# Optimization experiments

Hardware: AMD Instinct MI355X
Metric: run time of the kernel (lower is better)

Reference implementation:

```python
import jax, jax.numpy as jnp
import numpy as np

VL = 32

def setup_inputs() -> dict:
    key = jax.random.key(0)
    k1, k2, k3 = jax.random.split(key, 3)
    user = jax.random.normal(k1, (16384, 20, VL + 1), dtype=jnp.float32)
    ctx = jax.random.normal(k2, (16384, 10, VL + 1), dtype=jnp.float32)
    doc = jax.random.normal(k3, (16384, 30, VL + 1), dtype=jnp.float32)
    return {"user": user, "ctx": ctx, "doc": doc}

def reference(user, ctx, doc):
    # feats: [B, F, vl+1] where F = total field count across user/ctx/doc
    feats = jnp.concatenate([user, ctx, doc], axis=1)
    v = feats[..., :VL]          # [B, F, vl] latent factors
    linear = feats[..., -1]      # [B, F]   linear term (last column)
    # FM cross term: 0.5 * ((sum_f v)^2 - sum_f v^2), summed over latent dims
    sum_v = jnp.sum(v, axis=1)           # [B, vl]
    sum_v2 = jnp.sum(v * v, axis=1)      # [B, vl]
    cross = 0.5 * jnp.sum(sum_v * sum_v - sum_v2, axis=-1)  # [B]
    logits = cross + jnp.sum(linear, axis=1)                 # [B]
    return jax.nn.sigmoid(logits)
```

## Files before the change

kernel.cpp:

```cpp
#include <hip/hip_runtime.h>
#include <hip/hip_bf16.h>
#include <math.h>


#define NS 16384
#define NU 20
#define NC 10
#define ND 30
#define RW 33

__global__ __launch_bounds__(256) void fm_kernel(
    const float* __restrict__ user,
    const float* __restrict__ ctx,
    const float* __restrict__ doc,
    float* __restrict__ out) {
  const int tid   = blockIdx.x * blockDim.x + threadIdx.x;
  const int samp  = tid >> 5;
  const int lane  = tid & 31;

  const float* __restrict__ ub = user + (size_t)samp * (NU * RW);
  const float* __restrict__ cb = ctx  + (size_t)samp * (NC * RW);
  const float* __restrict__ db = doc  + (size_t)samp * (ND * RW);

  float lin = 0.f;
  if (lane < NU) lin += ub[lane * RW + 32];
  if (lane < NC) lin += cb[lane * RW + 32];
  if (lane < ND) lin += db[lane * RW + 32];

  float sv = 0.f, sv2 = 0.f;

#pragma unroll
  for (int f = 0; f < NU; ++f) {
    float x = ub[f * RW + lane];
    sv += x; sv2 = fmaf(x, x, sv2);
  }
#pragma unroll
  for (int f = 0; f < NC; ++f) {
    float x = cb[f * RW + lane];
    sv += x; sv2 = fmaf(x, x, sv2);
  }
#pragma unroll
  for (int f = 0; f < ND; ++f) {
    float x = db[f * RW + lane];
    sv += x; sv2 = fmaf(x, x, sv2);
  }

  float part = fmaf(sv, sv, -sv2);

#pragma unroll
  for (int m = 16; m > 0; m >>= 1) {
    part += __shfl_xor(part, m, 64);
    lin  += __shfl_xor(lin,  m, 64);
  }

  if (lane == 0) {
    float logit = fmaf(0.5f, part, lin);
    out[samp] = 1.f / (1.f + expf(-logit));
  }
}

extern "C" void kernel_launch(void* const* d_in, const int* in_sizes, int n_in,
                              void* d_out, int out_size, void* d_ws, size_t ws_size,
                              hipStream_t stream) {
  const float* user = (const float*)d_in[0];
  const float* ctx  = (const float*)d_in[1];
  const float* doc  = (const float*)d_in[2];
  float* out = (float*)d_out;

  dim3 block(256);
  dim3 grid(NS / 8);
  fm_kernel<<<grid, block, 0, stream>>>(user, ctx, doc, out);
}
```

Baseline: 153.5 us.

## Stage sample pairs through LDS with coalesced float4 loads per wavefront

Each 64-lane wavefront now handles two samples. It copies their contiguous user/ctx/doc rows into shared memory with aligned float4 loads, then each half-wave reduces one sample from LDS. The aim is to replace the strided 33-float-row global reads with fully coalesced wide loads. The cost is about 31.7 KB of LDS per 128-thread block, which limits occupancy, plus an extra pass through LDS. There is no barrier between the LDS store and load; this relies on each wavefront reading only data it wrote itself.

```diff
diff --git a/kernel.cpp b/kernel.cpp
--- a/kernel.cpp
+++ b/kernel.cpp
@@ -4,46 +4,77 @@
 
 
 #define NS 16384
-#define NU 20
-#define NC 10
-#define ND 30
 #define RW 33
 
-__global__ __launch_bounds__(256) void fm_kernel(
+__global__ __launch_bounds__(128) void fm_kernel(
     const float* __restrict__ user,
     const float* __restrict__ ctx,
     const float* __restrict__ doc,
     float* __restrict__ out) {
-  const int tid   = blockIdx.x * blockDim.x + threadIdx.x;
-  const int samp  = tid >> 5;
-  const int lane  = tid & 31;
+  __shared__ float smem[7920];
 
-  const float* __restrict__ ub = user + (size_t)samp * (NU * RW);
-  const float* __restrict__ cb = ctx  + (size_t)samp * (NC * RW);
-  const float* __restrict__ db = doc  + (size_t)samp * (ND * RW);
+  const int tid  = threadIdx.x;
+  const int w    = tid >> 6;
+  const int lane = tid & 63;
 
-  float lin = 0.f;
-  if (lane < NU) lin += ub[lane * RW + 32];
-  if (lane < NC) lin += cb[lane * RW + 32];
-  if (lane < ND) lin += db[lane * RW + 32];
+  float* lu = smem + w * 3960;
+  float* lc = lu + 1320;
+  float* ld = lc + 660;
 
-  float sv = 0.f, sv2 = 0.f;
+  const int spair = blockIdx.x * 4 + 2 * w;
+
+  const float4* gu = (const float4*)(user + (size_t)spair * 660);
+  const float4* gc = (const float4*)(ctx  + (size_t)spair * 330);
+  const float4* gd = (const float4*)(doc  + (size_t)spair * 990);
+
+  float4* su4 = (float4*)lu;
+  float4* sc4 = (float4*)lc;
+  float4* sd4 = (float4*)ld;
 
 #pragma unroll
-  for (int f = 0; f < NU; ++f) {
-    float x = ub[f * RW + lane];
+  for (int i = 0; i < 6; ++i) {
+    int idx = i * 64 + lane;
+    if (idx < 330) su4[idx] = gu[idx];
+  }
+#pragma unroll
+  for (int i = 0; i < 3; ++i) {
+    int idx = i * 64 + lane;
+    if (idx < 165) sc4[idx] = gc[idx];
+  }
+#pragma unroll
+  for (int i = 0; i < 8; ++i) {
+    int idx = i * 64 + lane;
+    if (idx < 495) sd4[idx] = gd[idx];
+  }
+
+  const int sel = lane >> 5;
+  const int e   = lane & 31;
+
+  const float* mu = lu + sel * 660;
+  const float* mc = lc + sel * 330;
+  const float* md = ld + sel * 990;
+
+  float sv = 0.f, sv2 = 0.f, lin = 0.f;
+
+#pragma unroll
+  for (int f = 0; f < 20; ++f) {
+    float x = mu[f * RW + e];
     sv += x; sv2 = fmaf(x, x, sv2);
   }
 #pragma unroll
-  for (int f = 0; f < NC; ++f) {
-    float x = cb[f * RW + lane];
+  for (int f = 0; f < 10; ++f) {
+    float x = mc[f * RW + e];
     sv += x; sv2 = fmaf(x, x, sv2);
   }
 #pragma unroll
-  for (int f = 0; f < ND; ++f) {
-    float x = db[f * RW + lane];
+  for (int f = 0; f < 30; ++f) {
+    float x = md[f * RW + e];
     sv += x; sv2 = fmaf(x, x, sv2);
   }
+
+  if (e < 20) lin += mu[e * RW + 32];
+  if (e < 10) lin += mc[e * RW + 32];
+  if (e < 30) lin += md[e * RW + 32];
 
   float part = fmaf(sv, sv, -sv2);
 
@@ -53,9 +84,9 @@
     lin  += __shfl_xor(lin,  m, 64);
   }
 
-  if (lane == 0) {
+  if (e == 0) {
     float logit = fmaf(0.5f, part, lin);
-    out[samp] = 1.f / (1.f + expf(-logit));
+    out[spair + sel] = 1.f / (1.f + expf(-logit));
   }
 }
 
@@ -67,7 +98,7 @@
   const float* doc  = (const float*)d_in[2];
   float* out = (float*)d_out;
 
-  dim3 block(256);
-  dim3 grid(NS / 8);
+  dim3 block(128);
+  dim3 grid(NS / 4);
   fm_kernel<<<grid, block, 0, stream>>>(user, ctx, doc, out);
 }
```

After: 144.8 us. -5.7%, faster.

## Stage sample rows via coalesced float4 loads into LDS, split fields across half-waves

Applied to the files above, without the earlier changes.

Each 128-thread block now loads two samples' user/ctx/doc rows with contiguous float4 global loads into shared memory. It then reduces from LDS, with each 64-lane wave handling one sample and the two half-waves splitting the field range. This replaces strided scalar global loads (stride 33 floats per field) with fully vectorized coalesced loads. The cost is a block barrier, about 15.8KB of LDS per block and smaller blocks.

```diff
diff --git a/kernel.cpp b/kernel.cpp
--- a/kernel.cpp
+++ b/kernel.cpp
@@ -4,58 +4,98 @@
 
 
 #define NS 16384
-#define NU 20
-#define NC 10
-#define ND 30
-#define RW 33
 
-__global__ __launch_bounds__(256) void fm_kernel(
+__global__ __launch_bounds__(128) void fm_kernel(
     const float* __restrict__ user,
     const float* __restrict__ ctx,
     const float* __restrict__ doc,
     float* __restrict__ out) {
-  const int tid   = blockIdx.x * blockDim.x + threadIdx.x;
-  const int samp  = tid >> 5;
-  const int lane  = tid & 31;
+  __shared__ float smem[3960];
 
-  const float* __restrict__ ub = user + (size_t)samp * (NU * RW);
-  const float* __restrict__ cb = ctx  + (size_t)samp * (NC * RW);
-  const float* __restrict__ db = doc  + (size_t)samp * (ND * RW);
+  const int tid = threadIdx.x;
+  const int spair = blockIdx.x * 2;
 
-  float lin = 0.f;
-  if (lane < NU) lin += ub[lane * RW + 32];
-  if (lane < NC) lin += cb[lane * RW + 32];
-  if (lane < ND) lin += db[lane * RW + 32];
+  const float4* gu = (const float4*)(user + (size_t)spair * 660);
+  const float4* gc = (const float4*)(ctx  + (size_t)spair * 330);
+  const float4* gd = (const float4*)(doc  + (size_t)spair * 990);
+  float4* su = (float4*)smem;
+  float4* sc = (float4*)(smem + 1320);
+  float4* sd = (float4*)(smem + 1980);
+
+  {
+    float4 r0 = gu[tid], r1 = gu[128 + tid];
+    float4 r2, r3, r4, r5, r6, r7;
+    bool pu = (256 + tid) < 330;
+    if (pu) r2 = gu[256 + tid];
+    r3 = gc[tid];
+    bool pc = (128 + tid) < 165;
+    if (pc) r4 = gc[128 + tid];
+    r5 = gd[tid];
+    r6 = gd[128 + tid];
+    r7 = gd[256 + tid];
+    bool pd = (384 + tid) < 495;
+    float4 r8;
+    if (pd) r8 = gd[384 + tid];
+
+    su[tid] = r0;
+    su[128 + tid] = r1;
+    if (pu) su[256 + tid] = r2;
+    sc[tid] = r3;
+    if (pc) sc[128 + tid] = r4;
+    sd[tid] = r5;
+    sd[128 + tid] = r6;
+    sd[256 + tid] = r7;
+    if (pd) sd[384 + tid] = r8;
+  }
+  __syncthreads();
+
+  const int w = tid >> 6;
+  const int l = tid & 63;
+  const int h = l >> 5;
+  const int e = l & 31;
+
+  const float* mu = smem + w * 660;
+  const float* mc = smem + 1320 + w * 330;
+  const float* md = smem + 1980 + w * 990;
+
+  const float* p1 = (h ? md : mu) + e;
+  const float* p2 = (h ? (md + 660) : mc) + e;
 
   float sv = 0.f, sv2 = 0.f;
-
 #pragma unroll
-  for (int f = 0; f < NU; ++f) {
-    float x = ub[f * RW + lane];
+  for (int f = 0; f < 20; ++f) {
+    float x = p1[f * 33];
     sv += x; sv2 = fmaf(x, x, sv2);
   }
 #pragma unroll
-  for (int f = 0; f < NC; ++f) {
-    float x = cb[f * RW + lane];
-    sv += x; sv2 = fmaf(x, x, sv2);
-  }
-#pragma unroll
-  for (int f = 0; f < ND; ++f) {
-    float x = db[f * RW + lane];
+  for (int f = 0; f < 10; ++f) {
+    float x = p2[f * 33];
     sv += x; sv2 = fmaf(x, x, sv2);
   }
 
-  float part = fmaf(sv, sv, -sv2);
+  float lin = 0.f;
+  if (h == 0) {
+    if (e < 20)      lin = mu[e * 33 + 32];
+    else if (e < 30) lin = mc[(e - 20) * 33 + 32];
+  } else {
+    if (e < 30)      lin = md[e * 33 + 32];
+  }
+
+  float svT  = sv  + __shfl_xor(sv,  32, 64);
+  float sv2T = sv2 + __shfl_xor(sv2, 32, 64);
+  float linT = lin + __shfl_xor(lin, 32, 64);
+
+  float part = fmaf(svT, svT, -sv2T);
 
 #pragma unroll
   for (int m = 16; m > 0; m >>= 1) {
     part += __shfl_xor(part, m, 64);
-    lin  += __shfl_xor(lin,  m, 64);
+    linT += __shfl_xor(linT, m, 64);
   }
 
-  if (lane == 0) {
-    float logit = fmaf(0.5f, part, lin);
-    out[samp] = 1.f / (1.f + expf(-logit));
+  if (l == 0) {
+    float logit = fmaf(0.5f, part, linT);
+    out[spair + w] = 1.f / (1.f + expf(-logit));
   }
 }
 
@@ -67,7 +107,7 @@
   const float* doc  = (const float*)d_in[2];
   float* out = (float*)d_out;
 
-  dim3 block(256);
-  dim3 grid(NS / 8);
+  dim3 block(128);
+  dim3 grid(NS / 2);
   fm_kernel<<<grid, block, 0, stream>>>(user, ctx, doc, out);
 }
```

Measured after the change: 142.6 us. 1.08x faster.

## Map one sample per wavefront with 4-wide vector loads across rows

Applied to the files above, without the earlier changes.

Restructures the FM kernel so each 64-lane wavefront handles one sample, with lanes split into 8 row groups by 8 column chunks that each load four floats at once. Per-lane load count drops from sixty scalar loads to about eight vector loads. The partial sums are then reduced across row groups and column chunks with shuffles. This aims to raise memory-level parallelism and use full wavefronts, at the cost of unaligned vector loads (rows are 33 floats) and more shuffle traffic.

```diff
diff --git a/kernel.cpp b/kernel.cpp
--- a/kernel.cpp
+++ b/kernel.cpp
@@ -1,61 +1,72 @@
 #include <hip/hip_runtime.h>
-#include <hip/hip_bf16.h>
 #include <math.h>
 
 
 #define NS 16384
-#define NU 20
-#define NC 10
-#define ND 30
-#define RW 33
 
-__global__ __launch_bounds__(256) void fm_kernel(
+typedef float f4u __attribute__((ext_vector_type(4), aligned(4)));
+
+__global__ __launch_bounds__(256, 4) void fm_kernel(
     const float* __restrict__ user,
     const float* __restrict__ ctx,
     const float* __restrict__ doc,
     float* __restrict__ out) {
-  const int tid   = blockIdx.x * blockDim.x + threadIdx.x;
-  const int samp  = tid >> 5;
-  const int lane  = tid & 31;
+  const int tid = threadIdx.x;
+  const int w   = tid >> 6;
+  const int l   = tid & 63;
+  const int s   = blockIdx.x * 4 + w;
 
-  const float* __restrict__ ub = user + (size_t)samp * (NU * RW);
-  const float* __restrict__ cb = ctx  + (size_t)samp * (NC * RW);
-  const float* __restrict__ db = doc  + (size_t)samp * (ND * RW);
+  const int k  = l & 7;
+  const int rg = l >> 3;
+
+  const float* __restrict__ ub = user + (size_t)s * 660;
+  const float* __restrict__ cb = ctx  + (size_t)s * 330;
+  const float* __restrict__ db = doc  + (size_t)s * 990;
+
+  auto rowptr = [&](int r) -> const float* {
+    return r < 20 ? ub + r * 33
+         : (r < 30 ? cb + (r - 20) * 33
+                   : db + (r - 30) * 33);
+  };
 
   float lin = 0.f;
-  if (lane < NU) lin += ub[lane * RW + 32];
-  if (lane < NC) lin += cb[lane * RW + 32];
-  if (lane < ND) lin += db[lane * RW + 32];
+  if (l < 60) lin = rowptr(l)[32];
 
-  float sv = 0.f, sv2 = 0.f;
+  float4 S = {0.f, 0.f, 0.f, 0.f};
+  float q = 0.f;
 
 #pragma unroll
-  for (int f = 0; f < NU; ++f) {
-    float x = ub[f * RW + lane];
-    sv += x; sv2 = fmaf(x, x, sv2);
-  }
-#pragma unroll
-  for (int f = 0; f < NC; ++f) {
-    float x = cb[f * RW + lane];
-    sv += x; sv2 = fmaf(x, x, sv2);
-  }
-#pragma unroll
-  for (int f = 0; f < ND; ++f) {
-    float x = db[f * RW + lane];
-    sv += x; sv2 = fmaf(x, x, sv2);
+  for (int j = 0; j < 8; ++j) {
+    const int r = 8 * j + rg;
+    if (j < 7 || rg < 4) {
+      const f4u x = *(const f4u*)(rowptr(r) + 4 * k);
+      S.x += x[0]; S.y += x[1]; S.z += x[2]; S.w += x[3];
+      q = fmaf(x[0], x[0], fmaf(x[1], x[1],
+          fmaf(x[2], x[2], fmaf(x[3], x[3], q))));
+    }
   }
 
-  float part = fmaf(sv, sv, -sv2);
+#pragma unroll
+  for (int m = 8; m <= 32; m <<= 1) {
+    S.x += __shfl_xor(S.x, m, 64);
+    S.y += __shfl_xor(S.y, m, 64);
+    S.z += __shfl_xor(S.z, m, 64);
+    S.w += __shfl_xor(S.w, m, 64);
+    q   += __shfl_xor(q,   m, 64);
+    lin += __shfl_xor(lin, m, 64);
+  }
+
+  float pp = S.x * S.x + S.y * S.y + S.z * S.z + S.w * S.w - q;
 
 #pragma unroll
-  for (int m = 16; m > 0; m >>= 1) {
-    part += __shfl_xor(part, m, 64);
-    lin  += __shfl_xor(lin,  m, 64);
+  for (int m = 1; m <= 4; m <<= 1) {
+    pp  += __shfl_xor(pp,  m, 64);
+    lin += __shfl_xor(lin, m, 64);
   }
 
-  if (lane == 0) {
-    float logit = fmaf(0.5f, part, lin);
-    out[samp] = 1.f / (1.f + expf(-logit));
+  if (l == 0) {
+    float logit = fmaf(0.5f, pp, lin);
+    out[s] = 1.f / (1.f + expf(-logit));
   }
 }
 
@@ -68,6 +79,6 @@
   float* out = (float*)d_out;
 
   dim3 block(256);
-  dim3 grid(NS / 8);
+  dim3 grid(NS / 4);
   fm_kernel<<<grid, block, 0, stream>>>(user, ctx, doc, out);
 }
```

Result: faster. 142.6 us (-7.1%).
